# Kernel tuning notes

Hardware: AMD Instinct MI355X
Metric: run time of the kernel (lower is better)

Reference implementation:

```python
import jax, jax.numpy as jnp
import numpy as np

IOU_TR = 0.3
SCORE_TR = 0.1
EPS = 1e-9
N_DET = 4096
N_CLASSES = 20


def setup_inputs() -> dict:
    key = jax.random.key(0)
    k1, k2, k3, k4 = jax.random.split(key, 4)
    scores = jax.random.uniform(k1, (N_DET,), dtype=jnp.float32)
    classes = jax.random.randint(k2, (N_DET,), 0, N_CLASSES).astype(jnp.float32)
    centers = jax.random.uniform(k3, (N_DET, 3), dtype=jnp.float32) * 64.0
    dims = jax.random.uniform(k4, (N_DET, 3), dtype=jnp.float32) * 8.0 + 1.0
    results = jnp.concatenate([scores[:, None], classes[:, None], centers, dims], axis=1)
    return {"results": results}


def _pairwise_iou3d(boxes):
    # boxes: [N, 6] = (cx, cy, cz, w, h, d) center format
    c = boxes[:, :3]
    d = boxes[:, 3:]
    lo = c - d * 0.5  # [N,3]
    hi = c + d * 0.5
    inter_lo = jnp.maximum(lo[:, None, :], lo[None, :, :])  # [N,N,3]
    inter_hi = jnp.minimum(hi[:, None, :], hi[None, :, :])
    inter = jnp.prod(jnp.clip(inter_hi - inter_lo, 0.0, None), axis=-1)  # [N,N]
    vol = jnp.prod(d, axis=-1)  # [N]
    union = vol[:, None] + vol[None, :] - inter
    return inter / (union + EPS)


def reference(results):
    # results: [N, 8] = (score, class, cx, cy, cz, w, h, d)
    N = results.shape[0]
    order = jnp.argsort(-results[:, 0])  # sort by score descending
    r = results[order]
    valid = r[:, 0] >= SCORE_TR  # score threshold filter
    iou = _pairwise_iou3d(r[:, 2:])  # [N,N]
    idx = jnp.arange(N)

    def body(i, state):
        keep, active = state
        cur = active[i]
        keep = keep.at[i].set(cur)
        # suppress later boxes whose IoU with box i exceeds threshold
        sup = cur & (iou[i] > IOU_TR) & (idx > i)
        active = active & (~sup)
        return keep, active

    keep, _ = jax.lax.fori_loop(0, N, body, (jnp.zeros(N, dtype=bool), valid))
    # static-shape output: suppressed / filtered rows zeroed instead of compacted
    return jnp.where(keep[:, None], r, jnp.zeros_like(r))
```

## Files before the change

kernel.cpp:

```cpp
#include <hip/hip_runtime.h>

typedef unsigned long long u64;
typedef unsigned int u32;
typedef unsigned short u16;

#define N_DET 4096
#define NW 64
#define IOU_TR 0.3f
#define SCORE_TR 0.1f
#define EPS 1e-9f


__device__ __forceinline__ u64 rl64(u64 v, int l) {
    unsigned lo = __builtin_amdgcn_readlane((unsigned)v, l);
    unsigned hi = __builtin_amdgcn_readlane((unsigned)(v >> 32), l);
    return ((u64)hi << 32) | lo;
}

__global__ void __launch_bounds__(256) k_sort(const float* __restrict__ res,
                                              float* __restrict__ rows,
                                              float* __restrict__ ssc,
                                              float4* __restrict__ soaLO,
                                              float4* __restrict__ soaHI,
                                              u64* __restrict__ A,
                                              u64* __restrict__ Trm) {
    __shared__ float s[N_DET];
    int tid = threadIdx.x;
    if (blockIdx.x == 0) {
        if (tid < 64) A[tid] = 0ull;
        if (tid >= 64 && tid < 128)
            Trm[(size_t)4095 * NW + (tid - 64)] = 0ull;
    }
    for (int j = tid; j < N_DET; j += 256) s[j] = res[j * 8];
    __syncthreads();
    int r = tid >> 4, c = tid & 15;
    int gi = blockIdx.x * 16 + r;
    float sc = s[gi];
    int part = 0;
    int j0 = c * 256;
    for (int j = j0; j < j0 + 256; ++j) {
        float sj = s[j];
        part += (sj > sc) || (sj == sc && j < gi);
    }
    part += __shfl_xor(part, 1, 64);
    part += __shfl_xor(part, 2, 64);
    part += __shfl_xor(part, 4, 64);
    part += __shfl_xor(part, 8, 64);
    if (c == 0) {
        int rank = part;
        float4 a = *(const float4*)(res + gi * 8);
        float4 b = *(const float4*)(res + gi * 8 + 4);
        *(float4*)(rows + rank * 8)     = a;
        *(float4*)(rows + rank * 8 + 4) = b;
        ssc[rank] = a.x;
        float cx = a.z, cy = a.w, cz = b.x, dx = b.y, dy = b.z, dz = b.w;
        soaLO[rank] = make_float4(cx - dx * 0.5f, cy - dy * 0.5f,
                                  cz - dz * 0.5f, (dx * dy) * dz);
        soaHI[rank] = make_float4(cx + dx * 0.5f, cy + dy * 0.5f,
                                  cz + dz * 0.5f, 0.0f);
    }
}

__global__ void k_sup(const float4* __restrict__ soaLO,
                      const float4* __restrict__ soaHI,
                      const float* __restrict__ ssc,
                      u64* __restrict__ Trm, u64* __restrict__ A) {
    int lane = threadIdx.x & 63;
    int wave = threadIdx.x >> 6;
    int i = blockIdx.x * 4 + wave;
    if (ssc[i] < SCORE_TR) return;
    float4 iLO = soaLO[i];
    float4 iHI = soaHI[i];
    u64 rowword = 0, rowOr = 0;
    for (int w = (i >> 6); w < NW; ++w) {
        int j = w * 64 + lane;
        float4 jLO = soaLO[j];
        float4 jHI = soaHI[j];
        float ix = fminf(iHI.x, jHI.x) - fmaxf(iLO.x, jLO.x); ix = fmaxf(ix, 0.f);
        float iy = fminf(iHI.y, jHI.y) - fmaxf(iLO.y, jLO.y); iy = fmaxf(iy, 0.f);
        float iz = fminf(iHI.z, jHI.z) - fmaxf(iLO.z, jLO.z); iz = fmaxf(iz, 0.f);
        float inter = (ix * iy) * iz;
        float uni = iLO.w + jLO.w - inter;
        float iou = inter / (uni + EPS);
        bool sb = (iou > IOU_TR) && (j > i);
        u64 m = __ballot(sb);
        rowOr |= m;
        rowword = (lane == w) ? m : rowword;
    }
    if (rowOr) {
        Trm[(size_t)i * NW + lane] = rowword;
        if (lane == 0) atomicOr(&A[i >> 6], 1ull << (i & 63));
    }
}

__global__ void __launch_bounds__(256, 1)
k_scan(const u64* __restrict__ Trm, const u64* __restrict__ A,
       const float* __restrict__ ssc, u64* __restrict__ keep) {
    __shared__ u64 s_valid[NW];
    __shared__ u16 s_nlist[4608];
    __shared__ int s_nsb;
    __shared__ u64 sbuf[2][48][64];
    const int tid = threadIdx.x;
    const int wv = tid >> 6;
    const int lane = tid & 63;

    for (int w = wv * 16; w < wv * 16 + 16; ++w) {
        float scw = ssc[w * 64 + lane];
        u64 m = __ballot(scw >= SCORE_TR);
        if (lane == 0) s_valid[w] = m;
    }
    __syncthreads();

    if (wv == 0) {
        u64 avA = A[lane] & s_valid[lane];
        int pc = __popcll(avA);
        int inc = pc;
#pragma unroll
        for (int d = 1; d < 64; d <<= 1) {
            int t = __shfl_up(inc, d, 64);
            if (lane >= d) inc += t;
        }
        int exc = inc - pc;
        int nTotal = __shfl(inc, 63, 64);
        u64 m = avA; int o = exc;
        while (m) {
            int k = __builtin_ctzll(m); m &= m - 1;
            s_nlist[o++] = (u16)(lane * 64 + k);
        }
        int nSB = (nTotal + 47) / 48;
        for (int t = nTotal + lane; t < (nSB + 1) * 48; t += 64)
            s_nlist[t] = (u16)4095;
        if (lane == 0) s_nsb = nSB;
    }
    __syncthreads();

    const int nSB = s_nsb;
    if (wv > 0 && nSB > 0) {
        const int base = (wv - 1) * 16;
#pragma unroll
        for (int s = 0; s < 16; ++s) {
            u32 si = (u32)s_nlist[base + s];
            sbuf[0][base + s][lane] = Trm[(size_t)si * NW + lane];
        }
    }
    u64 act = s_valid[lane];
    __syncthreads();

    for (int t = 0; t < nSB; ++t) {
        const int cur = t & 1;
        if (wv > 0) {
            const int base = (wv - 1) * 16;
            const int off = (t + 1) * 48 + base;
#pragma unroll
            for (int s = 0; s < 16; ++s) {
                u32 si = (u32)s_nlist[off + s];
                sbuf[cur ^ 1][base + s][lane] = Trm[(size_t)si * NW + lane];
            }
        } else {
            const int off = t * 48;
#pragma unroll
            for (int s = 0; s < 48; ++s) {
                u32 siv = (u32)s_nlist[off + s];
                u32 si = (u32)__builtin_amdgcn_readfirstlane((int)siv);
                u64 row = sbuf[cur][s][lane];
                u64 aw = rl64(act, (int)(si >> 6));
                u64 msk = 0ull - ((aw >> (si & 63u)) & 1ull);
                act &= ~(row & msk);
            }
        }
        __syncthreads();
    }
    if (wv == 0) keep[lane] = act;
}

__global__ void k_out(const float* __restrict__ rows,
                      const u64* __restrict__ keep,
                      float* __restrict__ out) {
    int i = blockIdx.x * 256 + threadIdx.x;
    bool kp = (keep[i >> 6] >> (i & 63)) & 1ull;
    float4 a = kp ? ((const float4*)rows)[i * 2]     : make_float4(0.f, 0.f, 0.f, 0.f);
    float4 b = kp ? ((const float4*)rows)[i * 2 + 1] : make_float4(0.f, 0.f, 0.f, 0.f);
    ((float4*)out)[i * 2]     = a;
    ((float4*)out)[i * 2 + 1] = b;
}

extern "C" void kernel_launch(void* const* d_in, const int* in_sizes, int n_in,
                              void* d_out, int out_size, void* d_ws, size_t ws_size,
                              hipStream_t stream) {
    const float* res = (const float*)d_in[0];
    float* out = (float*)d_out;

    float*  rows  = (float*)d_ws;
    float*  ssc   = rows + N_DET * 8;
    float4* soaLO = (float4*)(ssc + N_DET);
    float4* soaHI = soaLO + N_DET;
    u64*    A     = (u64*)(soaHI + N_DET);
    u64*    keep  = A + NW;
    u64*    Trm   = keep + NW;

    k_sort<<<N_DET / 16, 256, 0, stream>>>(res, rows, ssc, soaLO, soaHI, A, Trm);
    k_sup <<<N_DET / 4, 256, 0, stream>>>(soaLO, soaHI, ssc, Trm, A);
    k_scan<<<1, 256, 0, stream>>>(Trm, A, ssc, keep);
    k_out <<<16, 256, 0, stream>>>(rows, keep, out);
}
```

Before: 52.50 us.

## Share j-box tiles across waves via double-buffered LDS in suppression kernel

The suppression kernel now has the four waves of a block (four consecutive i rows) cooperatively load 4x64 j-boxes per step into shared memory, stored as structure-of-arrays, and each wave reads them from LDS. The next tile is prefetched into registers and written into a second buffer while the current tile is processed. This cuts redundant global loads of box data across waves and overlaps load latency with compute. In exchange it adds a __syncthreads per step, and invalid-score waves can no longer exit early because they must take part in the loads and barriers.

```diff
diff --git a/kernel.cpp b/kernel.cpp
--- a/kernel.cpp
+++ b/kernel.cpp
@@ -61,33 +61,72 @@
     }
 }
 
-__global__ void k_sup(const float4* __restrict__ soaLO,
-                      const float4* __restrict__ soaHI,
-                      const float* __restrict__ ssc,
-                      u64* __restrict__ Trm, u64* __restrict__ A) {
-    int lane = threadIdx.x & 63;
-    int wave = threadIdx.x >> 6;
-    int i = blockIdx.x * 4 + wave;
-    if (ssc[i] < SCORE_TR) return;
+__global__ void __launch_bounds__(256) k_sup(const float4* __restrict__ soaLO,
+                                             const float4* __restrict__ soaHI,
+                                             const float* __restrict__ ssc,
+                                             u64* __restrict__ Trm,
+                                             u64* __restrict__ A) {
+    __shared__ float s_b[2][7][4][64];
+    const int tid = threadIdx.x;
+    const int wv = tid >> 6;
+    const int lane = tid & 63;
+    const int i0 = blockIdx.x * 4;
+    const int i = i0 + wv;
+    const int w0 = i0 >> 6;
+    const bool valid = ssc[i] >= SCORE_TR;
     float4 iLO = soaLO[i];
     float4 iHI = soaHI[i];
     u64 rowword = 0, rowOr = 0;
-    for (int w = (i >> 6); w < NW; ++w) {
-        int j = w * 64 + lane;
-        float4 jLO = soaLO[j];
-        float4 jHI = soaHI[j];
-        float ix = fminf(iHI.x, jHI.x) - fmaxf(iLO.x, jLO.x); ix = fmaxf(ix, 0.f);
-        float iy = fminf(iHI.y, jHI.y) - fmaxf(iLO.y, jLO.y); iy = fmaxf(iy, 0.f);
-        float iz = fminf(iHI.z, jHI.z) - fmaxf(iLO.z, jLO.z); iz = fmaxf(iz, 0.f);
-        float inter = (ix * iy) * iz;
-        float uni = iLO.w + jLO.w - inter;
-        float iou = inter / (uni + EPS);
-        bool sb = (iou > IOU_TR) && (j > i);
-        u64 m = __ballot(sb);
-        rowOr |= m;
-        rowword = (lane == w) ? m : rowword;
-    }
-    if (rowOr) {
+
+    {
+        int j = w0 * 64 + tid;
+        int c = tid >> 6, l = tid & 63;
+        if (j < N_DET) {
+            float4 lo = soaLO[j], hi = soaHI[j];
+            s_b[0][0][c][l] = lo.x; s_b[0][1][c][l] = lo.y;
+            s_b[0][2][c][l] = lo.z; s_b[0][3][c][l] = lo.w;
+            s_b[0][4][c][l] = hi.x; s_b[0][5][c][l] = hi.y;
+            s_b[0][6][c][l] = hi.z;
+        }
+    }
+    __syncthreads();
+
+    for (int w = w0; w < NW; w += 4) {
+        const int cur = ((w - w0) >> 2) & 1;
+        const int jn = (w + 4) * 64 + tid;
+        const bool inb = jn < N_DET;
+        float4 nlo = make_float4(0.f, 0.f, 0.f, 0.f);
+        float4 nhi = make_float4(0.f, 0.f, 0.f, 0.f);
+        if (inb) { nlo = soaLO[jn]; nhi = soaHI[jn]; }
+
+        const int nc = (NW - w < 4) ? (NW - w) : 4;
+        for (int c = 0; c < nc; ++c) {
+            int jj = (w + c) * 64 + lane;
+            float lox = s_b[cur][0][c][lane], loy = s_b[cur][1][c][lane];
+            float loz = s_b[cur][2][c][lane], vol = s_b[cur][3][c][lane];
+            float hix = s_b[cur][4][c][lane], hiy = s_b[cur][5][c][lane];
+            float hiz = s_b[cur][6][c][lane];
+            float ix = fminf(iHI.x, hix) - fmaxf(iLO.x, lox); ix = fmaxf(ix, 0.f);
+            float iy = fminf(iHI.y, hiy) - fmaxf(iLO.y, loy); iy = fmaxf(iy, 0.f);
+            float iz = fminf(iHI.z, hiz) - fmaxf(iLO.z, loz); iz = fmaxf(iz, 0.f);
+            float inter = (ix * iy) * iz;
+            float uni = iLO.w + vol - inter;
+            float iou = inter / (uni + EPS);
+            u64 m = __ballot(iou > IOU_TR && jj > i);
+            rowOr |= m;
+            rowword = (lane == (w + c)) ? m : rowword;
+        }
+        if (inb) {
+            int c = tid >> 6, l = tid & 63;
+            s_b[cur ^ 1][0][c][l] = nlo.x; s_b[cur ^ 1][1][c][l] = nlo.y;
+            s_b[cur ^ 1][2][c][l] = nlo.z; s_b[cur ^ 1][3][c][l] = nlo.w;
+            s_b[cur ^ 1][4][c][l] = nhi.x; s_b[cur ^ 1][5][c][l] = nhi.y;
+            s_b[cur ^ 1][6][c][l] = nhi.z;
+        }
+        __syncthreads();
+    }
+
+    if (valid && rowOr) {
         Trm[(size_t)i * NW + lane] = rowword;
         if (lane == 0) atomicOr(&A[i >> 6], 1ull << (i & 63));
     }
```

New measurement: 49.27 us (median of 2 runs). 1.07x faster.
